# Kernel optimization log

Hardware: AMD Instinct MI355X
Metric: run time of the kernel (lower is better)

Reference implementation:

```python
import jax, jax.numpy as jnp
import numpy as np

N_NODES = 100000
N_EDGES = 1600000
IN_FEATS = 128
H1, H2 = 100, 200
OUT_FEATS = 64


def _glorot(key, shape):
    fan_in, fan_out = shape
    limit = float(np.sqrt(6.0 / (fan_in + fan_out)))
    return jax.random.uniform(key, shape, jnp.float32, -limit, limit)


def setup_inputs() -> dict:
    key = jax.random.key(0)
    ks = jax.random.split(key, 9)
    x = jax.random.normal(ks[0], (N_NODES, IN_FEATS), jnp.float32)
    edge_src = jax.random.randint(ks[1], (N_EDGES,), 0, N_NODES, jnp.int32)
    edge_dst = jax.random.randint(ks[2], (N_EDGES,), 0, N_NODES, jnp.int32)
    W1 = _glorot(ks[3], (IN_FEATS, H1)); b1 = jnp.zeros((H1,), jnp.float32)
    W2 = _glorot(ks[4], (H1, H2));       b2 = jnp.zeros((H2,), jnp.float32)
    W3 = _glorot(ks[5], (H2, OUT_FEATS)); b3 = jnp.zeros((OUT_FEATS,), jnp.float32)
    return {"x": x, "edge_src": edge_src, "edge_dst": edge_dst,
            "W1": W1, "b1": b1, "W2": W2, "b2": b2, "W3": W3, "b3": b3}


def _gcn_layer(h, src, dst, norm_src, norm_dst, W, b):
    # DGL GraphConv, norm='both': D_out^{-1/2} applied at src, sum-aggregate,
    # D_in^{-1/2} at dst, then dense linear + bias.
    h = h * norm_src[:, None]
    msgs = h[src]                                   # [E, d] gather
    agg = jax.ops.segment_sum(msgs, dst, num_segments=N_NODES)  # scatter-add
    agg = agg * norm_dst[:, None]
    return agg @ W + b


def reference(x, edge_src, edge_dst, W1, b1, W2, b2, W3, b3):
    ones = jnp.ones((N_EDGES,), jnp.float32)
    deg_out = jax.ops.segment_sum(ones, edge_src, num_segments=N_NODES)
    deg_in = jax.ops.segment_sum(ones, edge_dst, num_segments=N_NODES)
    norm_src = jax.lax.rsqrt(jnp.maximum(deg_out, 1.0))
    norm_dst = jax.lax.rsqrt(jnp.maximum(deg_in, 1.0))

    h = _gcn_layer(x, edge_src, edge_dst, norm_src, norm_dst, W1, b1)
    h = jax.nn.elu(h)
    h = _gcn_layer(h, edge_src, edge_dst, norm_src, norm_dst, W2, b2)
    h = jax.nn.elu(h)
    h = _gcn_layer(h, edge_src, edge_dst, norm_src, norm_dst, W3, b3)
    return jax.nn.sigmoid(h)
```

## Files before the change

kernel.cpp:

```cpp
#include <hip/hip_runtime.h>
#include <hip/hip_bf16.h>
#include <math.h>

#define NN 100000
#define NE 1600000

#define NBUCK 8
#define BSZ (NN / NBUCK)
#define CHUNKS 64
#define CH_E (NE / CHUNKS)
#define FILL_BLOCKS (NBUCK * CHUNKS)
#define GEMM_GRID ((NN / 16 + 3) / 4)

#define SCAN_BLK 256
#define NB_SCAN ((NN + SCAN_BLK - 1) / SCAN_BLK)

typedef float f32x4 __attribute__((ext_vector_type(4)));
typedef short s16x8 __attribute__((ext_vector_type(8)));
typedef unsigned short u16x4 __attribute__((ext_vector_type(4)));
typedef int i32x4 __attribute__((ext_vector_type(4)));

static inline int grid_for(long total, int block, long cap = 16384) {
    long b = (total + block - 1) / block;
    if (b > cap) b = cap;
    if (b < 1) b = 1;
    return (int)b;
}

__device__ __forceinline__ unsigned short f2b(float f) {
    __hip_bfloat16 h = __float2bfloat16(f);
    return __builtin_bit_cast(unsigned short, h);
}
__device__ __forceinline__ float b2f(unsigned short u) {
    unsigned int x = ((unsigned int)u) << 16;
    return __builtin_bit_cast(float, x);
}


__global__ __launch_bounds__(256) void partial_hist_kernel(
    const int* __restrict__ src, const int* __restrict__ dst,
    int* __restrict__ scratch)
{
    __shared__ int h[BSZ];
    int g = blockIdx.x & 7, c = blockIdx.x >> 3;
    int lo = g * BSZ;
    for (int i = threadIdx.x; i < BSZ; i += 256) h[i] = 0;
    __syncthreads();
    const i32x4* src4 = reinterpret_cast<const i32x4*>(src + c * CH_E);
    const i32x4* dst4 = reinterpret_cast<const i32x4*>(dst + c * CH_E);
    for (int i = threadIdx.x; i < CH_E / 4; i += 256) {
        i32x4 s4 = src4[i];
        i32x4 d4 = dst4[i];
#pragma unroll
        for (int j = 0; j < 4; ++j) {
            unsigned si = (unsigned)(s4[j] - lo);
            unsigned di = (unsigned)(d4[j] - lo);
            if (si < BSZ) atomicAdd(&h[si], 1);
            if (di < BSZ) atomicAdd(&h[di], 0x10000);
        }
    }
    __syncthreads();
    int* o = scratch + ((size_t)g * CHUNKS + c) * BSZ;
    for (int i = threadIdx.x; i < BSZ; i += 256) o[i] = h[i];
}

__global__ void reduce_hist_kernel(const int* __restrict__ scratch,
                                   float* __restrict__ ns, float* __restrict__ nd,
                                   int* __restrict__ cnt_dst) {
    int n = blockIdx.x * blockDim.x + threadIdx.x;
    if (n >= NN) return;
    int g = n / BSZ, i = n - g * BSZ;
    const int* p = scratch + (size_t)g * CHUNKS * BSZ + i;
    unsigned cs = 0, cd = 0;
#pragma unroll 8
    for (int c = 0; c < CHUNKS; ++c) {
        unsigned v = (unsigned)p[(size_t)c * BSZ];
        cs += v & 0xffffu;
        cd += v >> 16;
    }
    ns[n] = rsqrtf(fmaxf((float)cs, 1.0f));
    nd[n] = rsqrtf(fmaxf((float)cd, 1.0f));
    cnt_dst[n] = (int)cd;
}

__global__ void block_sum_kernel(const int* __restrict__ cnt, int* __restrict__ partials) {
    __shared__ int sm[SCAN_BLK];
    int i = blockIdx.x * SCAN_BLK + threadIdx.x;
    sm[threadIdx.x] = (i < NN) ? cnt[i] : 0;
    __syncthreads();
    for (int s = SCAN_BLK / 2; s > 0; s >>= 1) {
        if (threadIdx.x < s) sm[threadIdx.x] += sm[threadIdx.x + s];
        __syncthreads();
    }
    if (threadIdx.x == 0) partials[blockIdx.x] = sm[0];
}

__global__ void scan_partials_kernel(int* __restrict__ p) {
    __shared__ int sm[512];
    int tid = threadIdx.x;
    int v = (tid < NB_SCAN) ? p[tid] : 0;
    sm[tid] = v;
    __syncthreads();
    for (int off = 1; off < 512; off <<= 1) {
        int t = (tid >= off) ? sm[tid - off] : 0;
        __syncthreads();
        sm[tid] += t;
        __syncthreads();
    }
    if (tid < NB_SCAN) p[tid] = sm[tid] - v;
}

__global__ void block_scan_kernel(const int* __restrict__ cnt, const int* __restrict__ partials,
                                  int* __restrict__ row_ptr) {
    __shared__ int sm[SCAN_BLK];
    int i = blockIdx.x * SCAN_BLK + threadIdx.x;
    int v = (i < NN) ? cnt[i] : 0;
    sm[threadIdx.x] = v;
    __syncthreads();
    for (int off = 1; off < SCAN_BLK; off <<= 1) {
        int t = (threadIdx.x >= off) ? sm[threadIdx.x - off] : 0;
        __syncthreads();
        sm[threadIdx.x] += t;
        __syncthreads();
    }
    if (i < NN) {
        int excl = partials[blockIdx.x] + sm[threadIdx.x] - v;
        row_ptr[i] = excl;
        if (i == NN - 1) row_ptr[NN] = excl + v;
    }
}

__global__ void chunk_offs_kernel(int* __restrict__ scratch, const int* __restrict__ row_ptr) {
    int n = blockIdx.x * blockDim.x + threadIdx.x;
    if (n >= NN) return;
    int g = n / BSZ, i = n - g * BSZ;
    int* pd = scratch + (size_t)g * CHUNKS * BSZ + i;
    int base = row_ptr[n];
#pragma unroll 8
    for (int c = 0; c < CHUNKS; ++c) {
        unsigned cnt = ((unsigned)pd[(size_t)c * BSZ]) >> 16;
        pd[(size_t)c * BSZ] = base;
        base += (int)cnt;
    }
}


template <int K_REAL, int N_REAL, int NTILES>
__device__ __forceinline__ void repack_one(const float* __restrict__ W,
                                           unsigned short* __restrict__ Wf, int t) {
    int j = t & 7, lane = (t >> 3) & 63, frag = t >> 9;
    int kt = frag / NTILES, nt = frag - kt * NTILES;
    int k = kt * 32 + (lane >> 4) * 8 + j;
    int n = nt * 16 + (lane & 15);
    float v = (k < K_REAL && n < N_REAL) ? W[(size_t)k * N_REAL + n] : 0.0f;
    Wf[t] = f2b(v);
}

#define R1_N (28 * 512)
#define R2_N (56 * 512)
#define R3_N (28 * 512)

__global__ void prep_kernel(const float* __restrict__ W1, unsigned short* __restrict__ W1f,
                            const float* __restrict__ W2, unsigned short* __restrict__ W2f,
                            const float* __restrict__ W3, unsigned short* __restrict__ W3f,
                            const float* __restrict__ b2, float* __restrict__ b2p) {
    int t = blockIdx.x * blockDim.x + threadIdx.x;
    if (t < R1_N) {
        repack_one<128, 100, 7>(W1, W1f, t);
    } else if (t < R1_N + R2_N) {
        repack_one<100, 200, 14>(W2, W2f, t - R1_N);
    } else if (t < R1_N + R2_N + R3_N) {
        repack_one<200, 64, 4>(W3, W3f, t - R1_N - R2_N);
    } else if (t < R1_N + R2_N + R3_N + 224) {
        int i = t - R1_N - R2_N - R3_N;
        b2p[i] = (i < 200) ? b2[i] : 0.0f;
    }
}

template <int K_STEPS, int NTILES, int N_REAL, int EPI, int K_PAD, int AMODE>
__device__ __forceinline__ void gemm_body(
    int wave, int lane, const void* __restrict__ Aptr,
    const unsigned short* __restrict__ Wf, const float* __restrict__ rowscale,
    const float* __restrict__ bias, void* __restrict__ outv)
{
    int row0 = wave << 4;
    if (row0 >= NN) return;
    int r = lane & 15, half = lane >> 4;

    f32x4 acc[NTILES];
#pragma unroll
    for (int nt = 0; nt < NTILES; ++nt) acc[nt] = (f32x4)(0.0f);

#pragma unroll
    for (int kt = 0; kt < K_STEPS; ++kt) {
        s16x8 a;
        if (AMODE == 0) {
            const unsigned short* arow = (const unsigned short*)Aptr
                + (size_t)(row0 + r) * K_PAD + half * 8 + kt * 32;
            a = *reinterpret_cast<const s16x8*>(arow);
        } else {
            const float* arow = (const float*)Aptr
                + (size_t)(row0 + r) * K_PAD + half * 8 + kt * 32;
            f32x4 alo = *reinterpret_cast<const f32x4*>(arow);
            f32x4 ahi = *reinterpret_cast<const f32x4*>(arow + 4);
#pragma unroll
            for (int j = 0; j < 4; ++j) {
                a[j]     = (short)f2b(alo[j]);
                a[4 + j] = (short)f2b(ahi[j]);
            }
        }
#pragma unroll
        for (int nt = 0; nt < NTILES; ++nt) {
            s16x8 b = *reinterpret_cast<const s16x8*>(
                Wf + (((kt * NTILES + nt) << 9) | (lane << 3)));
            acc[nt] = __builtin_amdgcn_mfma_f32_16x16x32_bf16(a, b, acc[nt], 0, 0, 0);
        }
    }

    int colbase = lane & 15;
    float rs[4];
#pragma unroll
    for (int j = 0; j < 4; ++j) rs[j] = rowscale[row0 + half * 4 + j];

    if (EPI == 2) {
        unsigned short* out = (unsigned short*)outv;
#pragma unroll
        for (int nt = 0; nt < NTILES; ++nt) {
            int col = nt * 16 + colbase;
            if (col < N_REAL) {
#pragma unroll
                for (int j = 0; j < 4; ++j) {
                    int row = row0 + half * 4 + j;
                    out[(size_t)row * N_REAL + col] = f2b(acc[nt][j] * rs[j]);
                }
            }
        }
    } else {
        unsigned short* out = (unsigned short*)outv;
        const int NOUT = NTILES * 16;
#pragma unroll
        for (int nt = 0; nt < NTILES; ++nt) {
            int col = nt * 16 + colbase;
            float bv = bias[col];
#pragma unroll
            for (int j = 0; j < 4; ++j) {
                int row = row0 + half * 4 + j;
                float v = acc[nt][j] * rs[j] + bv;
                v = (v > 0.0f) ? v : expm1f(v);
                out[(size_t)row * NOUT + col] = f2b(v);
            }
        }
    }
}

template <int K_STEPS, int NTILES, int N_REAL, int EPI, int K_PAD, int AMODE>
__global__ __launch_bounds__(256) void gemm_kernel(
    const void* __restrict__ Aptr, const unsigned short* __restrict__ Wf,
    const float* __restrict__ rowscale, const float* __restrict__ bias,
    void* __restrict__ outv)
{
    int wave = blockIdx.x * (blockDim.x >> 6) + (threadIdx.x >> 6);
    gemm_body<K_STEPS, NTILES, N_REAL, EPI, K_PAD, AMODE>(
        wave, threadIdx.x & 63, Aptr, Wf, rowscale, bias, outv);
}

__global__ __launch_bounds__(256) void fill_gemm1_kernel(
    const int* __restrict__ src, const int* __restrict__ dst,
    const int* __restrict__ scratch, int* __restrict__ col_src,
    const float* __restrict__ x, const unsigned short* __restrict__ W1f,
    const float* __restrict__ ns, unsigned short* __restrict__ y1)
{
    __shared__ int off[BSZ];
    if (blockIdx.x < FILL_BLOCKS) {
        int g = blockIdx.x & 7, c = blockIdx.x >> 3;
        int lo = g * BSZ;
        const int* pd = scratch + ((size_t)g * CHUNKS + c) * BSZ;
        for (int i = threadIdx.x; i < BSZ; i += 256) off[i] = pd[i];
        __syncthreads();
        const i32x4* src4 = reinterpret_cast<const i32x4*>(src + c * CH_E);
        const i32x4* dst4 = reinterpret_cast<const i32x4*>(dst + c * CH_E);
        for (int i = threadIdx.x; i < CH_E / 4; i += 256) {
            i32x4 s4 = src4[i];
            i32x4 d4 = dst4[i];
#pragma unroll
            for (int j = 0; j < 4; ++j) {
                unsigned di = (unsigned)(d4[j] - lo);
                if (di < BSZ) {
                    int p = atomicAdd(&off[di], 1);
                    col_src[p] = s4[j];
                }
            }
        }
    } else {
        int bid = blockIdx.x - FILL_BLOCKS;
        int wave = bid * 4 + (threadIdx.x >> 6);
        gemm_body<4, 7, 100, 2, 128, 1>(wave, threadIdx.x & 63, x, W1f, ns, nullptr, y1);
    }
}


#define GACC8(yb, stride)                                                        \
    int i = start;                                                               \
    f32x4 a0 = (f32x4)(0.0f), a1 = (f32x4)(0.0f), a2 = (f32x4)(0.0f),            \
          a3 = (f32x4)(0.0f);                                                    \
    for (; i + 8 <= end; i += 8) {                                               \
        int s0 = col_src[i],     s1 = col_src[i + 1];                            \
        int s2 = col_src[i + 2], s3 = col_src[i + 3];                            \
        int s4 = col_src[i + 4], s5 = col_src[i + 5];                            \
        int s6 = col_src[i + 6], s7 = col_src[i + 7];                            \
        u16x4 v0 = *reinterpret_cast<const u16x4*>(yb + (size_t)s0 * stride + g * 4); \
        u16x4 v1 = *reinterpret_cast<const u16x4*>(yb + (size_t)s1 * stride + g * 4); \
        u16x4 v2 = *reinterpret_cast<const u16x4*>(yb + (size_t)s2 * stride + g * 4); \
        u16x4 v3 = *reinterpret_cast<const u16x4*>(yb + (size_t)s3 * stride + g * 4); \
        u16x4 v4 = *reinterpret_cast<const u16x4*>(yb + (size_t)s4 * stride + g * 4); \
        u16x4 v5 = *reinterpret_cast<const u16x4*>(yb + (size_t)s5 * stride + g * 4); \
        u16x4 v6 = *reinterpret_cast<const u16x4*>(yb + (size_t)s6 * stride + g * 4); \
        u16x4 v7 = *reinterpret_cast<const u16x4*>(yb + (size_t)s7 * stride + g * 4); \
        _Pragma("unroll")                                                        \
        for (int j = 0; j < 4; ++j) {                                            \
            a0[j] += b2f(v0[j]) + b2f(v4[j]);                                    \
            a1[j] += b2f(v1[j]) + b2f(v5[j]);                                    \
            a2[j] += b2f(v2[j]) + b2f(v6[j]);                                    \
            a3[j] += b2f(v3[j]) + b2f(v7[j]);                                    \
        }                                                                        \
    }                                                                            \
    for (; i + 4 <= end; i += 4) {                                               \
        int s0 = col_src[i], s1 = col_src[i + 1];                                \
        int s2 = col_src[i + 2], s3 = col_src[i + 3];                            \
        u16x4 v0 = *reinterpret_cast<const u16x4*>(yb + (size_t)s0 * stride + g * 4); \
        u16x4 v1 = *reinterpret_cast<const u16x4*>(yb + (size_t)s1 * stride + g * 4); \
        u16x4 v2 = *reinterpret_cast<const u16x4*>(yb + (size_t)s2 * stride + g * 4); \
        u16x4 v3 = *reinterpret_cast<const u16x4*>(yb + (size_t)s3 * stride + g * 4); \
        _Pragma("unroll")                                                        \
        for (int j = 0; j < 4; ++j) {                                            \
            a0[j] += b2f(v0[j]); a1[j] += b2f(v1[j]);                            \
            a2[j] += b2f(v2[j]); a3[j] += b2f(v3[j]);                            \
        }                                                                        \
    }                                                                            \
    for (; i < end; ++i) {                                                       \
        int s0 = col_src[i];                                                     \
        u16x4 v0 = *reinterpret_cast<const u16x4*>(yb + (size_t)s0 * stride + g * 4); \
        _Pragma("unroll")                                                        \
        for (int j = 0; j < 4; ++j) a0[j] += b2f(v0[j]);                         \
    }                                                                            \
    f32x4 acc;                                                                   \
    _Pragma("unroll")                                                            \
    for (int j = 0; j < 4; ++j) acc[j] = (a0[j] + a1[j]) + (a2[j] + a3[j]);

__global__ void gather1_kernel(const unsigned short* __restrict__ y, const int* __restrict__ row_ptr,
                               const int* __restrict__ col_src, const float* __restrict__ ns,
                               const float* __restrict__ nd, const float* __restrict__ bias,
                               unsigned short* __restrict__ out) {
    unsigned t = blockIdx.x * blockDim.x + threadIdx.x;
    if (t >= NN * 25u) return;
    unsigned n = t / 25u, g = t - n * 25u;
    int start = row_ptr[n], end = row_ptr[n + 1];
    GACC8(y, 100)
    f32x4 b4 = *reinterpret_cast<const f32x4*>(bias + g * 4);
    float ndv = nd[n], nsv = ns[n];
    u16x4 o;
#pragma unroll
    for (int j = 0; j < 4; ++j) {
        float v = acc[j] * ndv + b4[j];
        v = (v > 0.0f) ? v : expm1f(v);
        o[j] = f2b(v * nsv);
    }
    *reinterpret_cast<u16x4*>(out + (size_t)n * 100 + g * 4) = o;
}

__global__ void gather2_kernel(const unsigned short* __restrict__ y, const int* __restrict__ row_ptr,
                               const int* __restrict__ col_src, unsigned short* __restrict__ out) {
    unsigned t = blockIdx.x * blockDim.x + threadIdx.x;
    if (t >= NN * 32u) return;
    unsigned n = t >> 5, g = t & 31u;
    if (g >= 25u) {
        u16x4 z = (u16x4)(0);
        *reinterpret_cast<u16x4*>(out + (size_t)n * 128 + 100 + (g - 25u) * 4) = z;
        return;
    }
    int start = row_ptr[n], end = row_ptr[n + 1];
    GACC8(y, 100)
    u16x4 o;
#pragma unroll
    for (int j = 0; j < 4; ++j) o[j] = f2b(acc[j]);
    *reinterpret_cast<u16x4*>(out + (size_t)n * 128 + g * 4) = o;
}

__global__ void gather3_kernel(const unsigned short* __restrict__ y, const int* __restrict__ row_ptr,
                               const int* __restrict__ col_src, const float* __restrict__ nd,
                               const float* __restrict__ bias, float* __restrict__ out) {
    unsigned t = blockIdx.x * blockDim.x + threadIdx.x;
    if (t >= NN * 16u) return;
    unsigned n = t >> 4, g = t & 15u;
    int start = row_ptr[n], end = row_ptr[n + 1];
    GACC8(y, 64)
    f32x4 b4 = *reinterpret_cast<const f32x4*>(bias + g * 4);
    float ndv = nd[n];
    f32x4 o;
#pragma unroll
    for (int j = 0; j < 4; ++j) {
        float v = acc[j] * ndv + b4[j];
        o[j] = 1.0f / (1.0f + expf(-v));
    }
    *reinterpret_cast<f32x4*>(out + (size_t)n * 64 + g * 4) = o;
}


extern "C" void kernel_launch(void* const* d_in, const int* in_sizes, int n_in,
                              void* d_out, int out_size, void* d_ws, size_t ws_size,
                              hipStream_t stream) {
    const float* x    = (const float*)d_in[0];
    const int*   esrc = (const int*)d_in[1];
    const int*   edst = (const int*)d_in[2];
    const float* W1   = (const float*)d_in[3];
    const float* b1   = (const float*)d_in[4];
    const float* W2   = (const float*)d_in[5];
    const float* b2   = (const float*)d_in[6];
    const float* W3   = (const float*)d_in[7];
    const float* b3   = (const float*)d_in[8];
    float* out = (float*)d_out;

    char* base = (char*)d_ws;
    size_t off = 0;
    auto alloc = [&](size_t bytes) -> void* {
        void* p = base + off;
        off += (bytes + 255) & ~(size_t)255;
        return p;
    };
    void* region1 = alloc((size_t)NN * 128 * 2);
    void* region2 = alloc((size_t)NN * 224 * 2);
    void* region3 = alloc((size_t)NN * 100 * 2);
    float* ns       = (float*)alloc(NN * 4);
    float* nd       = (float*)alloc(NN * 4);
    int*   cnt_dst  = (int*)alloc(NN * 4);
    int*   row_ptr  = (int*)alloc((NN + 1) * 4);
    int*   col_src  = (int*)alloc((size_t)NE * 4);
    int*   partials = (int*)alloc(512 * 4);
    unsigned short* W1f = (unsigned short*)alloc(R1_N * 2);
    unsigned short* W2f = (unsigned short*)alloc(R2_N * 2);
    unsigned short* W3f = (unsigned short*)alloc(R3_N * 2);
    float* b2p = (float*)alloc(224 * 4);

    int* scratch          = (int*)region1;
    unsigned short* agg2b = (unsigned short*)region1;
    unsigned short* y3    = (unsigned short*)region1;
    unsigned short* y1    = (unsigned short*)region2;
    unsigned short* h2b   = (unsigned short*)region2;
    unsigned short* h1s   = (unsigned short*)region3;

    const int BLK = 256;

    prep_kernel<<<grid_for(R1_N + R2_N + R3_N + 224, BLK), BLK, 0, stream>>>(
        W1, W1f, W2, W2f, W3, W3f, b2, b2p);

    partial_hist_kernel<<<NBUCK * CHUNKS, 256, 0, stream>>>(esrc, edst, scratch);
    reduce_hist_kernel<<<grid_for(NN, BLK), BLK, 0, stream>>>(scratch, ns, nd, cnt_dst);
    block_sum_kernel<<<NB_SCAN, SCAN_BLK, 0, stream>>>(cnt_dst, partials);
    scan_partials_kernel<<<1, 512, 0, stream>>>(partials);
    block_scan_kernel<<<NB_SCAN, SCAN_BLK, 0, stream>>>(cnt_dst, partials, row_ptr);
    chunk_offs_kernel<<<grid_for(NN, BLK), BLK, 0, stream>>>(scratch, row_ptr);

    fill_gemm1_kernel<<<FILL_BLOCKS + GEMM_GRID, 256, 0, stream>>>(
        esrc, edst, scratch, col_src, x, W1f, ns, y1);

    gather1_kernel<<<grid_for((long)NN * 25, BLK, 1 << 30), BLK, 0, stream>>>(
        y1, row_ptr, col_src, ns, nd, b1, h1s);

    gather2_kernel<<<grid_for((long)NN * 32, BLK, 1 << 30), BLK, 0, stream>>>(
        h1s, row_ptr, col_src, agg2b);
    gemm_kernel<4, 14, 200, 1, 128, 0><<<GEMM_GRID, BLK, 0, stream>>>(agg2b, W2f, nd, b2p, h2b);

    gemm_kernel<7, 4, 64, 2, 224, 0><<<GEMM_GRID, BLK, 0, stream>>>(h2b, W3f, ns, nullptr, y3);
    gather3_kernel<<<grid_for((long)NN * 16, BLK, 1 << 30), BLK, 0, stream>>>(
        y3, row_ptr, col_src, nd, b3, out);
}
```

Baseline: 399.7 us.

## Fuse preprocessing kernels and widen gather loads to 16-byte vectors

```diff
diff --git a/kernel.cpp b/kernel.cpp
--- a/kernel.cpp
+++ b/kernel.cpp
@@ -15,9 +15,16 @@
 #define SCAN_BLK 256
 #define NB_SCAN ((NN + SCAN_BLK - 1) / SCAN_BLK)
 
+#define R1_N (28 * 512)
+#define R2_N (56 * 512)
+#define R3_N (28 * 512)
+#define PREP_TOTAL (R1_N + R2_N + R3_N + 224)
+#define PREP_BLOCKS ((PREP_TOTAL + 255) / 256)
+
 typedef float f32x4 __attribute__((ext_vector_type(4)));
 typedef short s16x8 __attribute__((ext_vector_type(8)));
 typedef unsigned short u16x4 __attribute__((ext_vector_type(4)));
+typedef unsigned short u16x8 __attribute__((ext_vector_type(8)));
 typedef int i32x4 __attribute__((ext_vector_type(4)));
 
 static inline int grid_for(long total, int block, long cap = 16384) {
@@ -36,12 +43,36 @@
     return __builtin_bit_cast(float, x);
 }
 
-
-__global__ __launch_bounds__(256) void partial_hist_kernel(
-    const int* __restrict__ src, const int* __restrict__ dst,
-    int* __restrict__ scratch)
+template <int K_REAL, int N_REAL, int NTILES>
+__device__ __forceinline__ void repack_one(const float* __restrict__ W,
+                                           unsigned short* __restrict__ Wf, int t) {
+    int j = t & 7, lane = (t >> 3) & 63, frag = t >> 9;
+    int kt = frag / NTILES, nt = frag - kt * NTILES;
+    int k = kt * 32 + (lane >> 4) * 8 + j;
+    int n = nt * 16 + (lane & 15);
+    float v = (k < K_REAL && n < N_REAL) ? W[(size_t)k * N_REAL + n] : 0.0f;
+    Wf[t] = f2b(v);
+}
+
+__global__ __launch_bounds__(256) void hist_prep_kernel(
+    const int* __restrict__ src, const int* __restrict__ dst, int* __restrict__ scratch,
+    const float* __restrict__ W1, unsigned short* __restrict__ W1f,
+    const float* __restrict__ W2, unsigned short* __restrict__ W2f,
+    const float* __restrict__ W3, unsigned short* __restrict__ W3f,
+    const float* __restrict__ b2, float* __restrict__ b2p)
 {
     __shared__ int h[BSZ];
+    if (blockIdx.x >= FILL_BLOCKS) {
+        int t = (blockIdx.x - FILL_BLOCKS) * 256 + threadIdx.x;
+        if (t < R1_N) repack_one<128, 100, 7>(W1, W1f, t);
+        else if (t < R1_N + R2_N) repack_one<100, 200, 14>(W2, W2f, t - R1_N);
+        else if (t < R1_N + R2_N + R3_N) repack_one<200, 64, 4>(W3, W3f, t - R1_N - R2_N);
+        else if (t < PREP_TOTAL) {
+            int i = t - R1_N - R2_N - R3_N;
+            b2p[i] = (i < 200) ? b2[i] : 0.0f;
+        }
+        return;
+    }
     int g = blockIdx.x & 7, c = blockIdx.x >> 3;
     int lo = g * BSZ;
     for (int i = threadIdx.x; i < BSZ; i += 256) h[i] = 0;
@@ -66,27 +97,26 @@
 
 __global__ void reduce_hist_kernel(const int* __restrict__ scratch,
                                    float* __restrict__ ns, float* __restrict__ nd,
-                                   int* __restrict__ cnt_dst) {
+                                   int* __restrict__ cnt_dst, int* __restrict__ partials) {
+    __shared__ int sm[SCAN_BLK];
     int n = blockIdx.x * blockDim.x + threadIdx.x;
-    if (n >= NN) return;
-    int g = n / BSZ, i = n - g * BSZ;
-    const int* p = scratch + (size_t)g * CHUNKS * BSZ + i;
-    unsigned cs = 0, cd = 0;
+    int cdv = 0;
+    if (n < NN) {
+        int g = n / BSZ, i = n - g * BSZ;
+        const int* p = scratch + (size_t)g * CHUNKS * BSZ + i;
+        unsigned cs = 0, cd = 0;
 #pragma unroll 8
-    for (int c = 0; c < CHUNKS; ++c) {
-        unsigned v = (unsigned)p[(size_t)c * BSZ];
-        cs += v & 0xffffu;
-        cd += v >> 16;
-    }
-    ns[n] = rsqrtf(fmaxf((float)cs, 1.0f));
-    nd[n] = rsqrtf(fmaxf((float)cd, 1.0f));
-    cnt_dst[n] = (int)cd;
-}
-
-__global__ void block_sum_kernel(const int* __restrict__ cnt, int* __restrict__ partials) {
-    __shared__ int sm[SCAN_BLK];
-    int i = blockIdx.x * SCAN_BLK + threadIdx.x;
-    sm[threadIdx.x] = (i < NN) ? cnt[i] : 0;
+        for (int c = 0; c < CHUNKS; ++c) {
+            unsigned v = (unsigned)p[(size_t)c * BSZ];
+            cs += v & 0xffffu;
+            cd += v >> 16;
+        }
+        ns[n] = rsqrtf(fmaxf((float)cs, 1.0f));
+        nd[n] = rsqrtf(fmaxf((float)cd, 1.0f));
+        cnt_dst[n] = (int)cd;
+        cdv = (int)cd;
+    }
+    sm[threadIdx.x] = cdv;
     __syncthreads();
     for (int s = SCAN_BLK / 2; s > 0; s >>= 1) {
         if (threadIdx.x < s) sm[threadIdx.x] += sm[threadIdx.x + s];
@@ -110,8 +140,8 @@
     if (tid < NB_SCAN) p[tid] = sm[tid] - v;
 }
 
-__global__ void block_scan_kernel(const int* __restrict__ cnt, const int* __restrict__ partials,
-                                  int* __restrict__ row_ptr) {
+__global__ void scan_offs_kernel(const int* __restrict__ cnt, const int* __restrict__ partials,
+                                 int* __restrict__ row_ptr, int* __restrict__ scratch) {
     __shared__ int sm[SCAN_BLK];
     int i = blockIdx.x * SCAN_BLK + threadIdx.x;
     int v = (i < NN) ? cnt[i] : 0;
@@ -127,57 +157,19 @@
         int excl = partials[blockIdx.x] + sm[threadIdx.x] - v;
         row_ptr[i] = excl;
         if (i == NN - 1) row_ptr[NN] = excl + v;
-    }
-}
-
-__global__ void chunk_offs_kernel(int* __restrict__ scratch, const int* __restrict__ row_ptr) {
-    int n = blockIdx.x * blockDim.x + threadIdx.x;
-    if (n >= NN) return;
-    int g = n / BSZ, i = n - g * BSZ;
-    int* pd = scratch + (size_t)g * CHUNKS * BSZ + i;
-    int base = row_ptr[n];
+        int g = i / BSZ, ii = i - g * BSZ;
+        int* pd = scratch + (size_t)g * CHUNKS * BSZ + ii;
+        int base = excl;
 #pragma unroll 8
-    for (int c = 0; c < CHUNKS; ++c) {
-        unsigned cnt = ((unsigned)pd[(size_t)c * BSZ]) >> 16;
-        pd[(size_t)c * BSZ] = base;
-        base += (int)cnt;
-    }
-}
-
-
-template <int K_REAL, int N_REAL, int NTILES>
-__device__ __forceinline__ void repack_one(const float* __restrict__ W,
-                                           unsigned short* __restrict__ Wf, int t) {
-    int j = t & 7, lane = (t >> 3) & 63, frag = t >> 9;
-    int kt = frag / NTILES, nt = frag - kt * NTILES;
-    int k = kt * 32 + (lane >> 4) * 8 + j;
-    int n = nt * 16 + (lane & 15);
-    float v = (k < K_REAL && n < N_REAL) ? W[(size_t)k * N_REAL + n] : 0.0f;
-    Wf[t] = f2b(v);
-}
-
-#define R1_N (28 * 512)
-#define R2_N (56 * 512)
-#define R3_N (28 * 512)
-
-__global__ void prep_kernel(const float* __restrict__ W1, unsigned short* __restrict__ W1f,
-                            const float* __restrict__ W2, unsigned short* __restrict__ W2f,
-                            const float* __restrict__ W3, unsigned short* __restrict__ W3f,
-                            const float* __restrict__ b2, float* __restrict__ b2p) {
-    int t = blockIdx.x * blockDim.x + threadIdx.x;
-    if (t < R1_N) {
-        repack_one<128, 100, 7>(W1, W1f, t);
-    } else if (t < R1_N + R2_N) {
-        repack_one<100, 200, 14>(W2, W2f, t - R1_N);
-    } else if (t < R1_N + R2_N + R3_N) {
-        repack_one<200, 64, 4>(W3, W3f, t - R1_N - R2_N);
-    } else if (t < R1_N + R2_N + R3_N + 224) {
-        int i = t - R1_N - R2_N - R3_N;
-        b2p[i] = (i < 200) ? b2[i] : 0.0f;
-    }
-}
-
-template <int K_STEPS, int NTILES, int N_REAL, int EPI, int K_PAD, int AMODE>
+        for (int c = 0; c < CHUNKS; ++c) {
+            unsigned cc = ((unsigned)pd[(size_t)c * BSZ]) >> 16;
+            pd[(size_t)c * BSZ] = base;
+            base += (int)cc;
+        }
+    }
+}
+
+template <int K_STEPS, int NTILES, int N_REAL, int OSTRIDE, int EPI, int K_PAD, int AMODE>
 __device__ __forceinline__ void gemm_body(
     int wave, int lane, const void* __restrict__ Aptr,
     const unsigned short* __restrict__ Wf, const float* __restrict__ rowscale,
@@ -222,8 +214,8 @@
 #pragma unroll
     for (int j = 0; j < 4; ++j) rs[j] = rowscale[row0 + half * 4 + j];
 
+    unsigned short* out = (unsigned short*)outv;
     if (EPI == 2) {
-        unsigned short* out = (unsigned short*)outv;
 #pragma unroll
         for (int nt = 0; nt < NTILES; ++nt) {
             int col = nt * 16 + colbase;
@@ -231,13 +223,11 @@
 #pragma unroll
                 for (int j = 0; j < 4; ++j) {
                     int row = row0 + half * 4 + j;
-                    out[(size_t)row * N_REAL + col] = f2b(acc[nt][j] * rs[j]);
+                    out[(size_t)row * OSTRIDE + col] = f2b(acc[nt][j] * rs[j]);
                 }
             }
         }
     } else {
-        unsigned short* out = (unsigned short*)outv;
-        const int NOUT = NTILES * 16;
 #pragma unroll
         for (int nt = 0; nt < NTILES; ++nt) {
             int col = nt * 16 + colbase;
@@ -247,20 +237,20 @@
                 int row = row0 + half * 4 + j;
                 float v = acc[nt][j] * rs[j] + bv;
                 v = (v > 0.0f) ? v : expm1f(v);
-                out[(size_t)row * NOUT + col] = f2b(v);
+                out[(size_t)row * OSTRIDE + col] = f2b(v);
             }
         }
     }
 }
 
-template <int K_STEPS, int NTILES, int N_REAL, int EPI, int K_PAD, int AMODE>
+template <int K_STEPS, int NTILES, int N_REAL, int OSTRIDE, int EPI, int K_PAD, int AMODE>
 __global__ __launch_bounds__(256) void gemm_kernel(
     const void* __restrict__ Aptr, const unsigned short* __restrict__ Wf,
     const float* __restrict__ rowscale, const float* __restrict__ bias,
     void* __restrict__ outv)
 {
     int wave = blockIdx.x * (blockDim.x >> 6) + (threadIdx.x >> 6);
-    gemm_body<K_STEPS, NTILES, N_REAL, EPI, K_PAD, AMODE>(
+    gemm_body<K_STEPS, NTILES, N_REAL, OSTRIDE, EPI, K_PAD, AMODE>(
         wave, threadIdx.x & 63, Aptr, Wf, rowscale, bias, outv);
 }
 
@@ -294,115 +284,158 @@
     } else {
         int bid = blockIdx.x - FILL_BLOCKS;
         int wave = bid * 4 + (threadIdx.x >> 6);
-        gemm_body<4, 7, 100, 2, 128, 1>(wave, threadIdx.x & 63, x, W1f, ns, nullptr, y1);
-    }
-}
-
-
-#define GACC8(yb, stride)                                                        \
+        gemm_body<4, 7, 100, 104, 2, 128, 1>(wave, threadIdx.x & 63, x, W1f, ns, nullptr, y1);
+    }
+}
+
+
+#define GW(yb, stride, cb)                                                       \
     int i = start;                                                               \
-    f32x4 a0 = (f32x4)(0.0f), a1 = (f32x4)(0.0f), a2 = (f32x4)(0.0f),            \
-          a3 = (f32x4)(0.0f);                                                    \
-    for (; i + 8 <= end; i += 8) {                                               \
-        int s0 = col_src[i],     s1 = col_src[i + 1];                            \
-        int s2 = col_src[i + 2], s3 = col_src[i + 3];                            \
-        int s4 = col_src[i + 4], s5 = col_src[i + 5];                            \
-        int s6 = col_src[i + 6], s7 = col_src[i + 7];                            \
-        u16x4 v0 = *reinterpret_cast<const u16x4*>(yb + (size_t)s0 * stride + g * 4); \
-        u16x4 v1 = *reinterpret_cast<const u16x4*>(yb + (size_t)s1 * stride + g * 4); \
-        u16x4 v2 = *reinterpret_cast<const u16x4*>(yb + (size_t)s2 * stride + g * 4); \
-        u16x4 v3 = *reinterpret_cast<const u16x4*>(yb + (size_t)s3 * stride + g * 4); \
-        u16x4 v4 = *reinterpret_cast<const u16x4*>(yb + (size_t)s4 * stride + g * 4); \
-        u16x4 v5 = *reinterpret_cast<const u16x4*>(yb + (size_t)s5 * stride + g * 4); \
-        u16x4 v6 = *reinterpret_cast<const u16x4*>(yb + (size_t)s6 * stride + g * 4); \
-        u16x4 v7 = *reinterpret_cast<const u16x4*>(yb + (size_t)s7 * stride + g * 4); \
+    f32x4 c0a=(f32x4)(0.f),c0b=(f32x4)(0.f),c1a=(f32x4)(0.f),c1b=(f32x4)(0.f);  \
+    f32x4 c2a=(f32x4)(0.f),c2b=(f32x4)(0.f),c3a=(f32x4)(0.f),c3b=(f32x4)(0.f);  \
+    for (; i + 4 <= end; i += 4) {                                               \
+        int s0=col_src[i],s1=col_src[i+1],s2=col_src[i+2],s3=col_src[i+3];       \
+        u16x8 v0=*reinterpret_cast<const u16x8*>(yb+(size_t)s0*stride+cb);       \
+        u16x8 v1=*reinterpret_cast<const u16x8*>(yb+(size_t)s1*stride+cb);       \
+        u16x8 v2=*reinterpret_cast<const u16x8*>(yb+(size_t)s2*stride+cb);       \
+        u16x8 v3=*reinterpret_cast<const u16x8*>(yb+(size_t)s3*stride+cb);       \
         _Pragma("unroll")                                                        \
-        for (int j = 0; j < 4; ++j) {                                            \
-            a0[j] += b2f(v0[j]) + b2f(v4[j]);                                    \
-            a1[j] += b2f(v1[j]) + b2f(v5[j]);                                    \
-            a2[j] += b2f(v2[j]) + b2f(v6[j]);                                    \
-            a3[j] += b2f(v3[j]) + b2f(v7[j]);                                    \
-        }                                                                        \
-    }                                                                            \
-    for (; i + 4 <= end; i += 4) {                                               \
-        int s0 = col_src[i], s1 = col_src[i + 1];                                \
-        int s2 = col_src[i + 2], s3 = col_src[i + 3];                            \
-        u16x4 v0 = *reinterpret_cast<const u16x4*>(yb + (size_t)s0 * stride + g * 4); \
-        u16x4 v1 = *reinterpret_cast<const u16x4*>(yb + (size_t)s1 * stride + g * 4); \
-        u16x4 v2 = *reinterpret_cast<const u16x4*>(yb + (size_t)s2 * stride + g * 4); \
-        u16x4 v3 = *reinterpret_cast<const u16x4*>(yb + (size_t)s3 * stride + g * 4); \
-        _Pragma("unroll")                                                        \
-        for (int j = 0; j < 4; ++j) {                                            \
-            a0[j] += b2f(v0[j]); a1[j] += b2f(v1[j]);                            \
-            a2[j] += b2f(v2[j]); a3[j] += b2f(v3[j]);                            \
+        for (int j=0;j<4;++j){                                                   \
+            c0a[j]+=b2f(v0[j]); c0b[j]+=b2f(v0[4+j]);                            \
+            c1a[j]+=b2f(v1[j]); c1b[j]+=b2f(v1[4+j]);                            \
+            c2a[j]+=b2f(v2[j]); c2b[j]+=b2f(v2[4+j]);                            \
+            c3a[j]+=b2f(v3[j]); c3b[j]+=b2f(v3[4+j]);                            \
         }                                                                        \
     }                                                                            \
     for (; i < end; ++i) {                                                       \
-        int s0 = col_src[i];                                                     \
-        u16x4 v0 = *reinterpret_cast<const u16x4*>(yb + (size_t)s0 * stride + g * 4); \
+        int s0=col_src[i];                                                       \
+        u16x8 v0=*reinterpret_cast<const u16x8*>(yb+(size_t)s0*stride+cb);       \
         _Pragma("unroll")                                                        \
-        for (int j = 0; j < 4; ++j) a0[j] += b2f(v0[j]);                         \
+        for (int j=0;j<4;++j){ c0a[j]+=b2f(v0[j]); c0b[j]+=b2f(v0[4+j]); }       \
     }                                                                            \
-    f32x4 acc;                                                                   \
+    float acc8[8];                                                               \
     _Pragma("unroll")                                                            \
-    for (int j = 0; j < 4; ++j) acc[j] = (a0[j] + a1[j]) + (a2[j] + a3[j]);
+    for (int j=0;j<4;++j){ acc8[j]=(c0a[j]+c1a[j])+(c2a[j]+c3a[j]);              \
+                           acc8[4+j]=(c0b[j]+c1b[j])+(c2b[j]+c3b[j]); }
+
+#define GT4(yb, stride, cb)                                                      \
+    int i = start;                                                               \
+    f32x4 t0=(f32x4)(0.f),t1=(f32x4)(0.f),t2=(f32x4)(0.f),t3=(f32x4)(0.f);      \
+    for (; i + 8 <= end; i += 8) {                                               \
+        int s0=col_src[i],s1=col_src[i+1],s2=col_src[i+2],s3=col_src[i+3];       \
+        int s4=col_src[i+4],s5=col_src[i+5],s6=col_src[i+6],s7=col_src[i+7];     \
+        u16x4 v0=*reinterpret_cast<const u16x4*>(yb+(size_t)s0*stride+cb);       \
+        u16x4 v1=*reinterpret_cast<const u16x4*>(yb+(size_t)s1*stride+cb);       \
+        u16x4 v2=*reinterpret_cast<const u16x4*>(yb+(size_t)s2*stride+cb);       \
+        u16x4 v3=*reinterpret_cast<const u16x4*>(yb+(size_t)s3*stride+cb);       \
+        u16x4 v4=*reinterpret_cast<const u16x4*>(yb+(size_t)s4*stride+cb);       \
+        u16x4 v5=*reinterpret_cast<const u16x4*>(yb+(size_t)s5*stride+cb);       \
+        u16x4 v6=*reinterpret_cast<const u16x4*>(yb+(size_t)s6*stride+cb);       \
+        u16x4 v7=*reinterpret_cast<const u16x4*>(yb+(size_t)s7*stride+cb);       \
+        _Pragma("unroll")                                                        \
+        for (int j=0;j<4;++j){                                                   \
+            t0[j]+=b2f(v0[j])+b2f(v4[j]); t1[j]+=b2f(v1[j])+b2f(v5[j]);          \
+            t2[j]+=b2f(v2[j])+b2f(v6[j]); t3[j]+=b2f(v3[j])+b2f(v7[j]);          \
+        }                                                                        \
+    }                                                                            \
+    for (; i < end; ++i) {                                                       \
+        int s0=col_src[i];                                                       \
+        u16x4 v0=*reinterpret_cast<const u16x4*>(yb+(size_t)s0*stride+cb);       \
+        _Pragma("unroll")                                                        \
+        for (int j=0;j<4;++j) t0[j]+=b2f(v0[j]);                                 \
+    }                                                                            \
+    f32x4 acc4;                                                                  \
+    _Pragma("unroll")                                                            \
+    for (int j=0;j<4;++j) acc4[j]=(t0[j]+t1[j])+(t2[j]+t3[j]);
 
 __global__ void gather1_kernel(const unsigned short* __restrict__ y, const int* __restrict__ row_ptr,
                                const int* __restrict__ col_src, const float* __restrict__ ns,
                                const float* __restrict__ nd, const float* __restrict__ bias,
                                unsigned short* __restrict__ out) {
     unsigned t = blockIdx.x * blockDim.x + threadIdx.x;
-    if (t >= NN * 25u) return;
-    unsigned n = t / 25u, g = t - n * 25u;
-    int start = row_ptr[n], end = row_ptr[n + 1];
-    GACC8(y, 100)
-    f32x4 b4 = *reinterpret_cast<const f32x4*>(bias + g * 4);
-    float ndv = nd[n], nsv = ns[n];
-    u16x4 o;
-#pragma unroll
-    for (int j = 0; j < 4; ++j) {
-        float v = acc[j] * ndv + b4[j];
-        v = (v > 0.0f) ? v : expm1f(v);
-        o[j] = f2b(v * nsv);
-    }
-    *reinterpret_cast<u16x4*>(out + (size_t)n * 100 + g * 4) = o;
+    if (t < NN * 12u) {
+        unsigned n = t / 12u, g = t - n * 12u;
+        int start = row_ptr[n], end = row_ptr[n + 1];
+        int cb = g * 8;
+        GW(y, 104, cb)
+        f32x4 ba = *reinterpret_cast<const f32x4*>(bias + cb);
+        f32x4 bb = *reinterpret_cast<const f32x4*>(bias + cb + 4);
+        float ndv = nd[n], nsv = ns[n];
+        u16x8 o;
+#pragma unroll
+        for (int j = 0; j < 4; ++j) {
+            float va = acc8[j] * ndv + ba[j];
+            va = (va > 0.0f) ? va : expm1f(va);
+            o[j] = f2b(va * nsv);
+            float vb = acc8[4 + j] * ndv + bb[j];
+            vb = (vb > 0.0f) ? vb : expm1f(vb);
+            o[4 + j] = f2b(vb * nsv);
+        }
+        *reinterpret_cast<u16x8*>(out + (size_t)n * 104 + cb) = o;
+    } else if (t < NN * 13u) {
+        unsigned n = t - NN * 12u;
+        int start = row_ptr[n], end = row_ptr[n + 1];
+        GT4(y, 104, 96)
+        float ndv = nd[n], nsv = ns[n];
+        u16x4 o;
+#pragma unroll
+        for (int j = 0; j < 4; ++j) {
+            float v = acc4[j] * ndv + bias[96 + j];
+            v = (v > 0.0f) ? v : expm1f(v);
+            o[j] = f2b(v * nsv);
+        }
+        *reinterpret_cast<u16x4*>(out + (size_t)n * 104 + 96) = o;
+    }
 }
 
 __global__ void gather2_kernel(const unsigned short* __restrict__ y, const int* __restrict__ row_ptr,
                                const int* __restrict__ col_src, unsigned short* __restrict__ out) {
     unsigned t = blockIdx.x * blockDim.x + threadIdx.x;
-    if (t >= NN * 32u) return;
-    unsigned n = t >> 5, g = t & 31u;
-    if (g >= 25u) {
-        u16x4 z = (u16x4)(0);
-        *reinterpret_cast<u16x4*>(out + (size_t)n * 128 + 100 + (g - 25u) * 4) = z;
-        return;
-    }
-    int start = row_ptr[n], end = row_ptr[n + 1];
-    GACC8(y, 100)
-    u16x4 o;
-#pragma unroll
-    for (int j = 0; j < 4; ++j) o[j] = f2b(acc[j]);
-    *reinterpret_cast<u16x4*>(out + (size_t)n * 128 + g * 4) = o;
+    if (t < NN * 12u) {
+        unsigned n = t / 12u, g = t - n * 12u;
+        int start = row_ptr[n], end = row_ptr[n + 1];
+        int cb = g * 8;
+        GW(y, 104, cb)
+        u16x8 o;
+#pragma unroll
+        for (int j = 0; j < 4; ++j) { o[j] = f2b(acc8[j]); o[4 + j] = f2b(acc8[4 + j]); }
+        *reinterpret_cast<u16x8*>(out + (size_t)n * 128 + cb) = o;
+    } else if (t < NN * 13u) {
+        unsigned n = t - NN * 12u;
+        int start = row_ptr[n], end = row_ptr[n + 1];
+        GT4(y, 104, 96)
+        u16x8 o = (u16x8)(0);
+#pragma unroll
+        for (int j = 0; j < 4; ++j) o[j] = f2b(acc4[j]);
+        unsigned short* rowp = out + (size_t)n * 128;
+        *reinterpret_cast<u16x8*>(rowp + 96) = o;
+        u16x8 z = (u16x8)(0);
+        *reinterpret_cast<u16x8*>(rowp + 104) = z;
+        *reinterpret_cast<u16x8*>(rowp + 112) = z;
+        *reinterpret_cast<u16x8*>(rowp + 120) = z;
+    }
 }
 
 __global__ void gather3_kernel(const unsigned short* __restrict__ y, const int* __restrict__ row_ptr,
                                const int* __restrict__ col_src, const float* __restrict__ nd,
                                const float* __restrict__ bias, float* __restrict__ out) {
     unsigned t = blockIdx.x * blockDim.x + threadIdx.x;
-    if (t >= NN * 16u) return;
-    unsigned n = t >> 4, g = t & 15u;
+    if (t >= NN * 8u) return;
+    unsigned n = t >> 3, g = t & 7u;
     int start = row_ptr[n], end = row_ptr[n + 1];
-    GACC8(y, 64)
-    f32x4 b4 = *reinterpret_cast<const f32x4*>(bias + g * 4);
+    int cb = g * 8;
+    GW(y, 64, cb)
+    f32x4 ba = *reinterpret_cast<const f32x4*>(bias + cb);
+    f32x4 bb = *reinterpret_cast<const f32x4*>(bias + cb + 4);
     float ndv = nd[n];
-    f32x4 o;
+    f32x4 oa, ob;
 #pragma unroll
     for (int j = 0; j < 4; ++j) {
-        float v = acc[j] * ndv + b4[j];
-        o[j] = 1.0f / (1.0f + expf(-v));
-    }
-    *reinterpret_cast<f32x4*>(out + (size_t)n * 64 + g * 4) = o;
+        oa[j] = 1.0f / (1.0f + expf(-(acc8[j] * ndv + ba[j])));
+        ob[j] = 1.0f / (1.0f + expf(-(acc8[4 + j] * ndv + bb[j])));
+    }
+    *reinterpret_cast<f32x4*>(out + (size_t)n * 64 + cb) = oa;
+    *reinterpret_cast<f32x4*>(out + (size_t)n * 64 + cb + 4) = ob;
 }
 
 
@@ -429,7 +462,7 @@
     };
     void* region1 = alloc((size_t)NN * 128 * 2);
     void* region2 = alloc((size_t)NN * 224 * 2);
-    void* region3 = alloc((size_t)NN * 100 * 2);
+    void* region3 = alloc((size_t)NN * 104 * 2);
     float* ns       = (float*)alloc(NN * 4);
     float* nd       = (float*)alloc(NN * 4);
     int*   cnt_dst  = (int*)alloc(NN * 4);
@@ -450,27 +483,25 @@
 
     const int BLK = 256;
 
-    prep_kernel<<<grid_for(R1_N + R2_N + R3_N + 224, BLK), BLK, 0, stream>>>(
-        W1, W1f, W2, W2f, W3, W3f, b2, b2p);
-
-    partial_hist_kernel<<<NBUCK * CHUNKS, 256, 0, stream>>>(esrc, edst, scratch);
-    reduce_hist_kernel<<<grid_for(NN, BLK), BLK, 0, stream>>>(scratch, ns, nd, cnt_dst);
-    block_sum_kernel<<<NB_SCAN, SCAN_BLK, 0, stream>>>(cnt_dst, partials);
+    hist_prep_kernel<<<FILL_BLOCKS + PREP_BLOCKS, 256, 0, stream>>>(
+        esrc, edst, scratch, W1, W1f, W2, W2f, W3, W3f, b2, b2p);
+    reduce_hist_kernel<<<NB_SCAN, SCAN_BLK, 0, stream>>>(scratch, ns, nd, cnt_dst, partials);
     scan_partials_kernel<<<1, 512, 0, stream>>>(partials);
-    block_scan_kernel<<<NB_SCAN, SCAN_BLK, 0, stream>>>(cnt_dst, partials, row_ptr);
-    chunk_offs_kernel<<<grid_for(NN, BLK), BLK, 0, stream>>>(scratch, row_ptr);
+    scan_offs_kernel<<<NB_SCAN, SCAN_BLK, 0, stream>>>(cnt_dst, partials, row_ptr, scratch);
 
     fill_gemm1_kernel<<<FILL_BLOCKS + GEMM_GRID, 256, 0, stream>>>(
         esrc, edst, scratch, col_src, x, W1f, ns, y1);
 
-    gather1_kernel<<<grid_for((long)NN * 25, BLK, 1 << 30), BLK, 0, stream>>>(
+    gather1_kernel<<<grid_for((long)NN * 13, BLK, 1 << 30), BLK, 0, stream>>>(
         y1, row_ptr, col_src, ns, nd, b1, h1s);
 
-    gather2_kernel<<<grid_for((long)NN * 32, BLK, 1 << 30), BLK, 0, stream>>>(
+    gather2_kernel<<<grid_for((long)NN * 13, BLK, 1 << 30), BLK, 0, stream>>>(
         h1s, row_ptr, col_src, agg2b);
-    gemm_kernel<4, 14, 200, 1, 128, 0><<<GEMM_GRID, BLK, 0, stream>>>(agg2b, W2f, nd, b2p, h2b);
-
-    gemm_kernel<7, 4, 64, 2, 224, 0><<<GEMM_GRID, BLK, 0, stream>>>(h2b, W3f, ns, nullptr, y3);
-    gather3_kernel<<<grid_for((long)NN * 16, BLK, 1 << 30), BLK, 0, stream>>>(
+    gemm_kernel<4, 14, 200, 224, 1, 128, 0><<<GEMM_GRID, BLK, 0, stream>>>(
+        agg2b, W2f, nd, b2p, h2b);
+
+    gemm_kernel<7, 4, 64, 64, 2, 224, 0><<<GEMM_GRID, BLK, 0, stream>>>(
+        h2b, W3f, ns, nullptr, y3);
+    gather3_kernel<<<grid_for((long)NN * 8, BLK, 1 << 30), BLK, 0, stream>>>(
         y3, row_ptr, col_src, nd, b3, out);
 }
```

After: 453.2 us. 13.4% more time.
